# Optimization experiments

Measured on AMD Instinct MI355X. Metric: run time of the kernel, lower is better.

The kernel has to match this reference:

```python
import jax, jax.numpy as jnp
import numpy as np

B, S, D = 2048, 8, 1280
K = 1                 # n_components_remove
HIGH_T = 0.6          # PC1_HIGH_ACTIVITY_THRESHOLD
STORM_T = 0.8         # solar_storm_threshold


def setup_inputs() -> dict:
    key = jax.random.key(0)
    k1, k2 = jax.random.split(key, 2)
    features = jax.random.normal(k1, (B, S, D), dtype=jnp.float32)
    kp_index = jax.random.uniform(k2, (B,), dtype=jnp.float32) * 9.0
    cmr_gate = jnp.ones((1,), dtype=jnp.float32)  # nn.Parameter(torch.ones(1))
    return {"features": features, "kp_index": kp_index, "cmr_gate": cmr_gate}


def reference(features, kp_index, cmr_gate):
    # Per-sample standardization over the feature axis (numpy std, ddof=0)
    mu = features.mean(axis=2, keepdims=True)            # (B, S, 1)
    sigma = features.std(axis=2, keepdims=True) + 1e-8   # (B, S, 1)
    fn = (features - mu) / sigma                         # (B, S, D)

    # Batched thin SVD of the (S, D) normalized feature matrix
    U, sv, Vt = jnp.linalg.svd(fn, full_matrices=False)  # (B,S,S), (B,S), (B,S,D)
    var = sv * sv
    pc1_ratio = var[:, 0] / (var.sum(axis=-1) + 1e-8)    # (B,)

    # solar_flag: 0 normal, 1 high activity, 2 storm
    solar_flag = (pc1_ratio >= HIGH_T).astype(jnp.int32) + (pc1_ratio >= STORM_T).astype(jnp.int32)

    # Rank-K reconstruction of the common-mode (solar) component
    low = jnp.einsum('bsk,bk,bkd->bsd', U[:, :, :K], sv[:, :K], Vt[:, :K, :])
    clean = (fn - low) * sigma + mu                      # de-normalized cleaned features

    # Kp-gating: amplify CMR when Kp >= 5
    kp_gate = 1.0 + 0.5 * (kp_index >= 5.0).astype(features.dtype)[:, None, None]
    clean = features + kp_gate * (clean - features)

    # Learnable gate
    gate = jax.nn.sigmoid(cmr_gate)[0]
    features_clean = features + gate * (clean - features)
    return features_clean, pc1_ratio, solar_flag
```

## Files before the change

### kernel.cpp

```cpp
#include <hip/hip_runtime.h>
#include <math.h>


#define SV 8
#define DV 1280
#define D4 320
#define BSTRIDE (SV*DV)
#define GSZ 136
#define WSS 17

typedef __attribute__((ext_vector_type(8))) short bf16x8;
typedef __attribute__((ext_vector_type(4))) float f32x4;

union BF8 { bf16x8 v; short s[8]; };

__device__ __forceinline__ short f2bf(float x) {
    unsigned u = __float_as_uint(x);
    return (short)((u + 0x7FFFu + ((u >> 16) & 1u)) >> 16);
}
__device__ __forceinline__ float bf2f(short h) {
    return __uint_as_float(((unsigned)(unsigned short)h) << 16);
}

__global__ __launch_bounds__(256)
void cmr_gram(const float* __restrict__ feat, float* __restrict__ gram)
{
    const int lane = threadIdx.x & 63;
    const int wid  = (blockIdx.x * 256 + threadIdx.x) >> 6;
    const int m    = lane & 15;
    const int quad = lane >> 4;
    const int bt   = m >> 3;
    const int row  = m & 7;

    const float* __restrict__ fb =
        feat + ((size_t)(wid * 2 + bt)) * BSTRIDE + (size_t)row * DV;

    BF8 ones;
#pragma unroll
    for (int j = 0; j < 8; ++j) ones.s[j] = (short)0x3F80;

    f32x4 accHH = {0.f, 0.f, 0.f, 0.f};
    f32x4 accHL = {0.f, 0.f, 0.f, 0.f};
    f32x4 accS  = {0.f, 0.f, 0.f, 0.f};

#pragma unroll 4
    for (int c = 0; c < 40; ++c) {
        const int k0 = c * 32 + quad * 8;
        const float4 x0 = *(const float4*)(fb + k0);
        const float4 x1 = *(const float4*)(fb + k0 + 4);
        float x[8] = {x0.x, x0.y, x0.z, x0.w, x1.x, x1.y, x1.z, x1.w};
        BF8 hi, lo;
#pragma unroll
        for (int j = 0; j < 8; ++j) {
            hi.s[j] = f2bf(x[j]);
            lo.s[j] = f2bf(x[j] - bf2f(hi.s[j]));
        }
        accHH = __builtin_amdgcn_mfma_f32_16x16x32_bf16(hi.v, hi.v,   accHH, 0, 0, 0);
        accHL = __builtin_amdgcn_mfma_f32_16x16x32_bf16(hi.v, lo.v,   accHL, 0, 0, 0);
        accS  = __builtin_amdgcn_mfma_f32_16x16x32_bf16(hi.v, ones.v, accS,  0, 0, 0);
        accS  = __builtin_amdgcn_mfma_f32_16x16x32_bf16(lo.v, ones.v, accS,  0, 0, 0);
    }

    const int colb = (lane & 15) >> 3;
    const int col  = lane & 7;
#pragma unroll
    for (int r = 0; r < 4; ++r) {
        const int rowg = quad * 4 + r;
        if ((rowg >> 3) == colb) {
            float* gb = gram + ((size_t)(wid * 2 + colb)) * GSZ;
            gb[(rowg & 7) * 8 + col]      = accHH[r];
            gb[64 + (rowg & 7) * 8 + col] = accHL[r];
        }
    }
    if ((lane & 15) == 0) {
#pragma unroll
        for (int r = 0; r < 4; ++r) {
            const int rowg = quad * 4 + r;
            gram[((size_t)(wid * 2 + (rowg >> 3))) * GSZ + 128 + (rowg & 7)] = accS[r];
        }
    }
}

__global__ __launch_bounds__(64, 1)
void cmr_eigen(const float* __restrict__ gram,
               const float* __restrict__ kp,
               const float* __restrict__ cmr_gate,
               float* __restrict__ coef,
               float* __restrict__ out,
               int Bn)
{
    const int b = blockIdx.x * 64 + threadIdx.x;
    const float* __restrict__ g = gram + (size_t)b * GSZ;

    float G[8][8], S[8], mu[8], sig[8], rsig[8];
#pragma unroll
    for (int i = 0; i < 8; ++i) {
#pragma unroll
        for (int j = 0; j < 8; ++j)
            G[i][j] = g[i * 8 + j] + g[64 + i * 8 + j] + g[64 + j * 8 + i];
        S[i] = g[128 + i];
    }
    const float invD = 1.f / (float)DV;
#pragma unroll
    for (int i = 0; i < 8; ++i) {
        mu[i] = S[i] * invD;
        const float var = fmaxf(G[i][i] * invD - mu[i] * mu[i], 0.f);
        sig[i]  = sqrtf(var) + 1e-8f;
        rsig[i] = 1.f / sig[i];
    }
#pragma unroll
    for (int i = 0; i < 8; ++i)
#pragma unroll
        for (int j = 0; j < 8; ++j)
            G[i][j] = (G[i][j] - (float)DV * mu[i] * mu[j]) * rsig[i] * rsig[j];

    float tr = 0.f;
#pragma unroll
    for (int i = 0; i < 8; ++i) tr += G[i][i];

    float A[8][8];
    {
        const float rt = 1.f / fmaxf(tr, 1e-30f);
#pragma unroll
        for (int i = 0; i < 8; ++i)
#pragma unroll
            for (int j = 0; j < 8; ++j) A[i][j] = G[i][j] * rt;
    }
#pragma unroll
    for (int t = 0; t < 12; ++t) {
        float Bm[8][8];
        float trB = 0.f;
#pragma unroll
        for (int i = 0; i < 8; ++i)
#pragma unroll
            for (int j = i; j < 8; ++j) {
                float acc = 0.f;
#pragma unroll
                for (int k = 0; k < 8; ++k)
                    acc = fmaf(A[i][k], A[j][k], acc);
                Bm[i][j] = acc;
                if (i == j) trB += acc;
            }
        const float rt = 1.f / fmaxf(trB, 1e-30f);
#pragma unroll
        for (int i = 0; i < 8; ++i)
#pragma unroll
            for (int j = i; j < 8; ++j) {
                const float v = Bm[i][j] * rt;
                A[i][j] = v; A[j][i] = v;
            }
    }
    int bj = 0; float best = A[0][0];
#pragma unroll
    for (int k = 1; k < 8; ++k)
        if (A[k][k] > best) { best = A[k][k]; bj = k; }
    float u[8];
#pragma unroll
    for (int i = 0; i < 8; ++i) {
        float v = A[i][0];
#pragma unroll
        for (int k = 1; k < 8; ++k) v = (bj == k) ? A[i][k] : v;
        u[i] = v;
    }
    {
        float nn = 0.f;
#pragma unroll
        for (int i = 0; i < 8; ++i) nn = fmaf(u[i], u[i], nn);
        const float r = rsqrtf(fmaxf(nn, 1e-30f));
#pragma unroll
        for (int i = 0; i < 8; ++i) u[i] *= r;
    }
#pragma unroll
    for (int it = 0; it < 2; ++it) {
        float y[8]; float ny = 0.f;
#pragma unroll
        for (int i = 0; i < 8; ++i) {
            float acc = 0.f;
#pragma unroll
            for (int k = 0; k < 8; ++k) acc = fmaf(G[i][k], u[k], acc);
            y[i] = acc; ny = fmaf(acc, acc, ny);
        }
        const float r = rsqrtf(fmaxf(ny, 1e-30f));
#pragma unroll
        for (int i = 0; i < 8; ++i) u[i] = y[i] * r;
    }
    float lam = 0.f;
#pragma unroll
    for (int i = 0; i < 8; ++i) {
        float acc = 0.f;
#pragma unroll
        for (int k = 0; k < 8; ++k) acc = fmaf(G[i][k], u[k], acc);
        lam = fmaf(u[i], acc, lam);
    }
    const float pc1 = lam / (tr + 1e-8f);

    const float gate = 1.f / (1.f + expf(-cmr_gate[0]));
    const float kpg  = (kp[b] >= 5.0f) ? 1.5f : 1.0f;
    const float Gt   = gate * kpg;

    float bc = 0.f;
#pragma unroll
    for (int i = 0; i < 8; ++i) bc = fmaf(u[i] * rsig[i], mu[i], bc);

    float* wsb = coef + (size_t)b * WSS;
#pragma unroll
    for (int i = 0; i < 8; ++i) {
        wsb[i]     = u[i] * rsig[i];
        wsb[8 + i] = Gt * sig[i] * u[i];
    }
    wsb[16] = bc;
    out[(size_t)Bn * BSTRIDE + b] = pc1;
    out[(size_t)Bn * BSTRIDE + Bn + b] =
        (pc1 >= 0.6f ? 1.f : 0.f) + (pc1 >= 0.8f ? 1.f : 0.f);
}

__global__ __launch_bounds__(320)
void cmr_apply(const float* __restrict__ feat,
               const float* __restrict__ coef,
               float* __restrict__ out)
{
    const int tid  = threadIdx.x;
    const int lane = tid & 63;
    const int wq   = tid >> 6;
    const int b    = blockIdx.x;

    const float* __restrict__ wsb = coef + (size_t)b * WSS;
    float a[8], c[8];
#pragma unroll
    for (int s = 0; s < 8; ++s) { a[s] = wsb[s]; c[s] = wsb[8 + s]; }
    const float bc = wsb[16];

    const float4* __restrict__ f4 = (const float4*)(feat + (size_t)b * BSTRIDE);
    float4* __restrict__ o4 = (float4*)(out + (size_t)b * BSTRIDE);
    const int d4 = wq * 64 + lane;

    float4 f[8];
#pragma unroll
    for (int s = 0; s < 8; ++s) f[s] = f4[s * D4 + d4];

    float4 p = make_float4(-bc, -bc, -bc, -bc);
#pragma unroll
    for (int s = 0; s < 8; ++s) {
        p.x = fmaf(a[s], f[s].x, p.x);
        p.y = fmaf(a[s], f[s].y, p.y);
        p.z = fmaf(a[s], f[s].z, p.z);
        p.w = fmaf(a[s], f[s].w, p.w);
    }
#pragma unroll
    for (int s = 0; s < 8; ++s) {
        float4 o;
        o.x = fmaf(-c[s], p.x, f[s].x);
        o.y = fmaf(-c[s], p.y, f[s].y);
        o.z = fmaf(-c[s], p.z, f[s].z);
        o.w = fmaf(-c[s], p.w, f[s].w);
        o4[s * D4 + d4] = o;
    }
}

extern "C" void kernel_launch(void* const* d_in, const int* in_sizes, int n_in,
                              void* d_out, int out_size, void* d_ws, size_t ws_size,
                              hipStream_t stream) {
    const float* feat = (const float*)d_in[0];
    const float* kp   = (const float*)d_in[1];
    const float* gate = (const float*)d_in[2];
    float* out = (float*)d_out;
    const int Bn = in_sizes[0] / BSTRIDE;

    float* gram = (float*)d_ws;
    float* coef = gram + (size_t)Bn * GSZ;

    cmr_gram <<<Bn / 8,  256, 0, stream>>>(feat, gram);
    cmr_eigen<<<Bn / 64, 64,  0, stream>>>(gram, kp, gate, coef, out, Bn);
    cmr_apply<<<Bn,      320, 0, stream>>>(feat, coef, out);
}
```

Measured before the change: 175.5 us.

## Split Gram reduction across four waves per batch pair and use packed bf16 convert

The Gram/MFMA kernel now splits the 1280-wide reduction into four chunks, each handled by a separate wave, which launches four times more waves so the memory-bound read of features has more parallelism. Partial Gram matrices are written to a larger workspace and summed in the eigen kernel. The manual bf16 hi/lo split is also replaced with the hardware v_cvt_pk_bf16_f32 instruction to cut ALU work. The cost is extra workspace traffic and more work in the eigen kernel's load phase.

```diff
diff --git a/kernel.cpp b/kernel.cpp
--- a/kernel.cpp
+++ b/kernel.cpp
@@ -7,53 +7,56 @@
 #define D4 320
 #define BSTRIDE (SV*DV)
 #define GSZ 136
+#define SPLIT 4
+#define CITER (40/SPLIT)
 #define WSS 17
 
 typedef __attribute__((ext_vector_type(8))) short bf16x8;
 typedef __attribute__((ext_vector_type(4))) float f32x4;
 
-union BF8 { bf16x8 v; short s[8]; };
-
-__device__ __forceinline__ short f2bf(float x) {
-    unsigned u = __float_as_uint(x);
-    return (short)((u + 0x7FFFu + ((u >> 16) & 1u)) >> 16);
-}
-__device__ __forceinline__ float bf2f(short h) {
-    return __uint_as_float(((unsigned)(unsigned short)h) << 16);
-}
+union BF8 { bf16x8 v; short s[8]; unsigned u[4]; };
 
 __global__ __launch_bounds__(256)
 void cmr_gram(const float* __restrict__ feat, float* __restrict__ gram)
 {
     const int lane = threadIdx.x & 63;
     const int wid  = (blockIdx.x * 256 + threadIdx.x) >> 6;
+    const int pair = wid >> 2;
+    const int h    = wid & (SPLIT - 1);
     const int m    = lane & 15;
     const int quad = lane >> 4;
     const int bt   = m >> 3;
     const int row  = m & 7;
 
     const float* __restrict__ fb =
-        feat + ((size_t)(wid * 2 + bt)) * BSTRIDE + (size_t)row * DV;
+        feat + ((size_t)(pair * 2 + bt)) * BSTRIDE + (size_t)row * DV;
 
     BF8 ones;
 #pragma unroll
-    for (int j = 0; j < 8; ++j) ones.s[j] = (short)0x3F80;
+    for (int j = 0; j < 4; ++j) ones.u[j] = 0x3F803F80u;
 
     f32x4 accHH = {0.f, 0.f, 0.f, 0.f};
     f32x4 accHL = {0.f, 0.f, 0.f, 0.f};
     f32x4 accS  = {0.f, 0.f, 0.f, 0.f};
 
-#pragma unroll 4
-    for (int c = 0; c < 40; ++c) {
-        const int k0 = c * 32 + quad * 8;
+#pragma unroll
+    for (int c = 0; c < CITER; ++c) {
+        const int k0 = (h * CITER + c) * 32 + quad * 8;
         const float4 x0 = *(const float4*)(fb + k0);
         const float4 x1 = *(const float4*)(fb + k0 + 4);
         float x[8] = {x0.x, x0.y, x0.z, x0.w, x1.x, x1.y, x1.z, x1.w};
         BF8 hi, lo;
 #pragma unroll
-        for (int j = 0; j < 8; ++j) {
-            hi.s[j] = f2bf(x[j]);
-            lo.s[j] = f2bf(x[j] - bf2f(hi.s[j]));
+        for (int j = 0; j < 4; ++j) {
+            unsigned hp, lp;
+            asm("v_cvt_pk_bf16_f32 %0, %1, %2" : "=v"(hp) : "v"(x[2*j]), "v"(x[2*j+1]));
+            const float h0 = __uint_as_float(hp << 16);
+            const float h1 = __uint_as_float(hp & 0xFFFF0000u);
+            const float l0 = x[2*j]     - h0;
+            const float l1 = x[2*j + 1] - h1;
+            asm("v_cvt_pk_bf16_f32 %0, %1, %2" : "=v"(lp) : "v"(l0), "v"(l1));
+            hi.u[j] = hp;
+            lo.u[j] = lp;
         }
         accHH = __builtin_amdgcn_mfma_f32_16x16x32_bf16(hi.v, hi.v,   accHH, 0, 0, 0);
         accHL = __builtin_amdgcn_mfma_f32_16x16x32_bf16(hi.v, lo.v,   accHL, 0, 0, 0);
@@ -67,7 +70,7 @@
     for (int r = 0; r < 4; ++r) {
         const int rowg = quad * 4 + r;
         if ((rowg >> 3) == colb) {
-            float* gb = gram + ((size_t)(wid * 2 + colb)) * GSZ;
+            float* gb = gram + ((size_t)((pair * 2 + colb) * SPLIT + h)) * GSZ;
             gb[(rowg & 7) * 8 + col]      = accHH[r];
             gb[64 + (rowg & 7) * 8 + col] = accHL[r];
         }
@@ -76,7 +79,8 @@
 #pragma unroll
         for (int r = 0; r < 4; ++r) {
             const int rowg = quad * 4 + r;
-            gram[((size_t)(wid * 2 + (rowg >> 3))) * GSZ + 128 + (rowg & 7)] = accS[r];
+            gram[((size_t)((pair * 2 + (rowg >> 3)) * SPLIT + h)) * GSZ
+                 + 128 + (rowg & 7)] = accS[r];
         }
     }
 }
@@ -90,15 +94,25 @@
                int Bn)
 {
     const int b = blockIdx.x * 64 + threadIdx.x;
-    const float* __restrict__ g = gram + (size_t)b * GSZ;
+    const float* __restrict__ g = gram + (size_t)b * (GSZ * SPLIT);
 
     float G[8][8], S[8], mu[8], sig[8], rsig[8];
 #pragma unroll
     for (int i = 0; i < 8; ++i) {
 #pragma unroll
-        for (int j = 0; j < 8; ++j)
-            G[i][j] = g[i * 8 + j] + g[64 + i * 8 + j] + g[64 + j * 8 + i];
-        S[i] = g[128 + i];
+        for (int j = 0; j < 8; ++j) G[i][j] = 0.f;
+        S[i] = 0.f;
+    }
+#pragma unroll
+    for (int hh = 0; hh < SPLIT; ++hh) {
+        const float* __restrict__ gh = g + hh * GSZ;
+#pragma unroll
+        for (int i = 0; i < 8; ++i) {
+#pragma unroll
+            for (int j = 0; j < 8; ++j)
+                G[i][j] += gh[i * 8 + j] + gh[64 + i * 8 + j] + gh[64 + j * 8 + i];
+            S[i] += gh[128 + i];
+        }
     }
     const float invD = 1.f / (float)DV;
 #pragma unroll
@@ -267,9 +281,9 @@
     const int Bn = in_sizes[0] / BSTRIDE;
 
     float* gram = (float*)d_ws;
-    float* coef = gram + (size_t)Bn * GSZ;
-
-    cmr_gram <<<Bn / 8,  256, 0, stream>>>(feat, gram);
+    float* coef = gram + (size_t)Bn * GSZ * SPLIT;
+
+    cmr_gram <<<(Bn / 8) * SPLIT, 256, 0, stream>>>(feat, gram);
     cmr_eigen<<<Bn / 64, 64,  0, stream>>>(gram, kp, gate, coef, out, Bn);
     cmr_apply<<<Bn,      320, 0, stream>>>(feat, coef, out);
 }
```

Measured after the change: 181.7 us. 1.04x slower.
